# Kernel tuning notes

Measured on AMD Instinct MI355X. Metric: run time of the kernel, lower is better.

## Reference

```python
import jax, jax.numpy as jnp
import numpy as np

D_MODEL = 256
N_HEADS = 8
N_LEVELS = 4
N_POINTS = 4
HEAD_DIM = D_MODEL // N_HEADS
SPATIAL = [(64, 64), (32, 32), (16, 16), (8, 8)]
LEN_IN = sum(h * w for h, w in SPATIAL)
BATCH = 4
LEN_Q = LEN_IN


def _offset_bias():
    # replicate the module's _reset_parameters grid init for sampling_offsets.bias
    th = np.arange(N_HEADS, dtype=np.float64) * (2.0 * np.pi / N_HEADS)
    g = np.stack([np.cos(th), np.sin(th)], -1)
    g = g / np.abs(g).max(-1, keepdims=True)
    g = np.tile(g[:, None, None, :], (1, N_LEVELS, N_POINTS, 1))
    g = g * (np.arange(N_POINTS) + 1)[None, None, :, None]
    return jnp.asarray(g.reshape(-1), jnp.float32)


def setup_inputs() -> dict:
    key = jax.random.key(0)
    ks = jax.random.split(key, 10)
    s = 1.0 / np.sqrt(D_MODEL)
    return {
        "query": jax.random.normal(ks[0], (BATCH, LEN_Q, D_MODEL), jnp.float32),
        "reference_points": jax.random.uniform(ks[1], (BATCH, LEN_Q, N_LEVELS, 2), jnp.float32),
        "input_flatten": jax.random.normal(ks[2], (BATCH, LEN_IN, D_MODEL), jnp.float32),
        "input_spatial_shapes": np.array(SPATIAL, dtype=np.int64),
        "input_level_start_index": np.cumsum([0] + [h * w for h, w in SPATIAL[:-1]]).astype(np.int64),
        "W_val": jax.random.normal(ks[3], (D_MODEL, D_MODEL), jnp.float32) * s,
        "b_val": jnp.zeros((D_MODEL,), jnp.float32),
        "W_off": jax.random.normal(ks[4], (D_MODEL, N_HEADS * N_LEVELS * N_POINTS * 2), jnp.float32) * 0.01,
        "b_off": _offset_bias(),
        "W_attn": jax.random.normal(ks[5], (D_MODEL, N_HEADS * N_LEVELS * N_POINTS), jnp.float32) * 0.01,
        "b_attn": jnp.zeros((N_HEADS * N_LEVELS * N_POINTS,), jnp.float32),
        "W_out": jax.random.normal(ks[6], (D_MODEL, D_MODEL), jnp.float32) * s,
        "b_out": jnp.zeros((D_MODEL,), jnp.float32),
    }


def bilinear_sample(v, grid):
    # v: [B, C, H, W]; grid: [B, Q, P, 2] normalized to [-1, 1] (x=W axis, y=H axis)
    # matches torch F.grid_sample(mode='bilinear', padding_mode='zeros', align_corners=False)
    B, C, H, W = v.shape
    x = (grid[..., 0] + 1.0) * (W * 0.5) - 0.5
    y = (grid[..., 1] + 1.0) * (H * 0.5) - 0.5
    x0 = jnp.floor(x)
    y0 = jnp.floor(y)
    wx = x - x0
    wy = y - y0
    v_flat = v.reshape(B, C, H * W)

    def corner(xi, yi, wgt):
        valid = (xi >= 0) & (xi <= W - 1) & (yi >= 0) & (yi <= H - 1)
        xc = jnp.clip(xi, 0, W - 1).astype(jnp.int32)
        yc = jnp.clip(yi, 0, H - 1).astype(jnp.int32)
        idx = (yc * W + xc).reshape(B, 1, -1)
        g = jnp.take_along_axis(v_flat, jnp.broadcast_to(idx, (B, C, idx.shape[-1])), axis=2)
        return g * (wgt * valid).reshape(B, 1, -1)

    out = (corner(x0, y0, (1 - wx) * (1 - wy))
           + corner(x0 + 1, y0, wx * (1 - wy))
           + corner(x0, y0 + 1, (1 - wx) * wy)
           + corner(x0 + 1, y0 + 1, wx * wy))
    return out.reshape(B, C, grid.shape[1], grid.shape[2])


def reference(query, reference_points, input_flatten, input_spatial_shapes,
              input_level_start_index, W_val, b_val, W_off, b_off,
              W_attn, b_attn, W_out, b_out):
    ss = np.asarray(input_spatial_shapes)  # static [L, 2] (H, W)
    Nb, Lq, _ = query.shape
    value = (input_flatten @ W_val + b_val).reshape(Nb, -1, N_HEADS, HEAD_DIM)
    off = (query @ W_off + b_off).reshape(Nb, Lq, N_HEADS, N_LEVELS, N_POINTS, 2)
    attn = (query @ W_attn + b_attn).reshape(Nb, Lq, N_HEADS, N_LEVELS * N_POINTS)
    attn = jax.nn.softmax(attn, -1).reshape(Nb, Lq, N_HEADS, N_LEVELS, N_POINTS)
    # offset normalizer: (W, H) per level
    normalizer = jnp.asarray(ss[:, ::-1].copy(), jnp.float32)
    loc = reference_points[:, :, None, :, None, :] + off / normalizer[None, None, None, :, None, :]
    grids = 2.0 * loc - 1.0  # [N, Lq, H, L, P, 2]
    splits = np.cumsum([int(h) * int(w) for h, w in ss])[:-1]
    value_list = jnp.split(value, splits, axis=1)
    out = jnp.zeros((Nb * N_HEADS, HEAD_DIM, Lq), query.dtype)
    for lid, (h, w) in enumerate(ss):
        h, w = int(h), int(w)
        v = value_list[lid].transpose(0, 2, 3, 1).reshape(Nb * N_HEADS, HEAD_DIM, h, w)
        g = grids[:, :, :, lid].transpose(0, 2, 1, 3, 4).reshape(Nb * N_HEADS, Lq, N_POINTS, 2)
        sampled = bilinear_sample(v, g)  # [N*H, D, Lq, P]
        aw = attn[:, :, :, lid].transpose(0, 2, 1, 3).reshape(Nb * N_HEADS, 1, Lq, N_POINTS)
        out = out + (sampled * aw).sum(-1)
    out = out.reshape(Nb, N_HEADS * HEAD_DIM, Lq).transpose(0, 2, 1)
    return out @ W_out + b_out
```

## Files before the change

### kernel.cpp

```cpp
#include <hip/hip_runtime.h>
#include <hip/hip_bf16.h>
#include <math.h>

typedef unsigned short ushort_t;
typedef __attribute__((ext_vector_type(8))) short bf16x8;
typedef __attribute__((ext_vector_type(4))) float f32x4;

constexpr int BATCH   = 4;
constexpr int D_MODEL = 256;
constexpr int LEN_IN  = 5440;
constexpr int LEN_Q   = 5440;
constexpr int M_TOT   = BATCH * LEN_Q;

#define ASG __attribute__((address_space(1)))
#define ASL __attribute__((address_space(3)))

__device__ __forceinline__ void gld16(const void* g, void* l) {
    __builtin_amdgcn_global_load_lds((ASG const void*)g, (ASL void*)l, 16, 0, 0);
}

__device__ __forceinline__ ushort_t bfbits(float x) {
    __hip_bfloat16 h = __float2bfloat16(x);
    ushort_t u; __builtin_memcpy(&u, &h, 2); return u;
}
__device__ __forceinline__ unsigned pk2(float a, float b) {
    return (unsigned)bfbits(a) | ((unsigned)bfbits(b) << 16);
}

__global__ __launch_bounds__(256) void pack_inputs(
    const float* __restrict__ inflat, const float* __restrict__ query,
    const float* __restrict__ Wv, const float* __restrict__ Wo,
    const float* __restrict__ Wa, const float* __restrict__ Wout,
    const float* __restrict__ b_off, const float* __restrict__ b_attn,
    ushort_t* __restrict__ in_bf, ushort_t* __restrict__ q_bf,
    ushort_t* __restrict__ wvT, ushort_t* __restrict__ woaT,
    ushort_t* __restrict__ woutT, float* __restrict__ bias_oa)
{
    const int blk = blockIdx.x, tid = threadIdx.x;
    if (blk < 5440) {
        const float* src = (blk < 2720) ? inflat : query;
        ushort_t*    dst = (blk < 2720) ? in_bf : q_bf;
        const int rb = (blk < 2720) ? blk : blk - 2720;
        const size_t base = (size_t)rb * 2048 + tid * 8;
        float4 a = *(const float4*)(src + base);
        float4 b = *(const float4*)(src + base + 4);
        uint4 o;
        o.x = pk2(a.x, a.y); o.y = pk2(a.z, a.w);
        o.z = pk2(b.x, b.y); o.w = pk2(b.z, b.w);
        *(uint4*)(dst + base) = o;
    } else if (blk < 5504) {
        const float* src = (blk < 5472) ? Wv : Wout;
        ushort_t*    dst = (blk < 5472) ? wvT : woutT;
        const int base = (blk - ((blk < 5472) ? 5440 : 5472)) * 2048;
#pragma unroll
        for (int i = 0; i < 8; i++) {
            const int idx = base + i * 256 + tid;
            const int k = idx >> 8, n = idx & 255;
            dst[n * 256 + k] = bfbits(src[idx]);
        }
    } else if (blk < 5552) {
        const int base = (blk - 5504) * 2048;
#pragma unroll
        for (int i = 0; i < 8; i++) {
            const int idx = base + i * 256 + tid;
            const int k = idx / 384, j = idx - k * 384;
            const float v = (j < 256) ? Wo[k * 256 + j] : Wa[k * 128 + (j - 256)];
            woaT[j * 256 + k] = bfbits(v);
        }
    } else {
        bias_oa[tid] = b_off[tid];
        if (tid < 128) bias_oa[256 + tid] = b_attn[tid];
    }
}

template <bool OUT_BF16>
__device__ __forceinline__ void gemm_core(
    const ushort_t* __restrict__ A, const ushort_t* __restrict__ BT,
    const float* __restrict__ bias, void* __restrict__ Cp, int N,
    int bm, int bn, ushort_t* As, ushort_t* Bs)
{
    const int tid  = threadIdx.x;
    const int wave = tid >> 6, lane = tid & 63;
    const int wm = (wave >> 1) * 64, wn = (wave & 1) * 64;
    const int c0 = 2 * wave, c1 = 2 * wave + 1;
    const int kb = (lane & 3) * 8;
    const ushort_t* gA0 = A  + (size_t)(bm + c0 * 16 + (lane >> 2)) * 256 + kb;
    const ushort_t* gA1 = A  + (size_t)(bm + c1 * 16 + (lane >> 2)) * 256 + kb;
    const ushort_t* gB0 = BT + (size_t)(bn + c0 * 16 + (lane >> 2)) * 256 + kb;
    const ushort_t* gB1 = BT + (size_t)(bn + c1 * 16 + (lane >> 2)) * 256 + kb;
    ushort_t* lA0 = As + c0 * 512;
    ushort_t* lA1 = As + c1 * 512;
    ushort_t* lB0 = Bs + c0 * 512;
    ushort_t* lB1 = Bs + c1 * 512;

    f32x4 acc[4][4] = {};

    const int row = lane & 15, kg = (lane >> 4) * 8;
    for (int kt = 0; kt < 8; kt++) {
        gld16(gA0, lA0); gld16(gA1, lA1);
        gld16(gB0, lB0); gld16(gB1, lB1);
        gA0 += 32; gA1 += 32; gB0 += 32; gB1 += 32;
        __syncthreads();
        bf16x8 af[4], bfr[4];
#pragma unroll
        for (int i = 0; i < 4; i++)
            af[i] = *(const bf16x8*)(As + (wm + i * 16 + row) * 32 + kg);
#pragma unroll
        for (int j = 0; j < 4; j++)
            bfr[j] = *(const bf16x8*)(Bs + (wn + j * 16 + row) * 32 + kg);
#pragma unroll
        for (int i = 0; i < 4; i++)
#pragma unroll
            for (int j = 0; j < 4; j++)
                acc[i][j] = __builtin_amdgcn_mfma_f32_16x16x32_bf16(
                    af[i], bfr[j], acc[i][j], 0, 0, 0);
        __syncthreads();
    }

    const int col = lane & 15, rbase = (lane >> 4) * 4;
#pragma unroll
    for (int j = 0; j < 4; j++) {
        const int cc = bn + wn + j * 16 + col;
        const float bv = bias[cc];
#pragma unroll
        for (int i = 0; i < 4; i++) {
            const int rr = bm + wm + i * 16 + rbase;
#pragma unroll
            for (int r = 0; r < 4; r++) {
                const float v = acc[i][j][r] + bv;
                if (OUT_BF16) ((ushort_t*)Cp)[(size_t)(rr + r) * N + cc] = bfbits(v);
                else          ((float*)Cp)[(size_t)(rr + r) * N + cc] = v;
            }
        }
    }
}

__global__ __launch_bounds__(256) void gemm_dual(
    const ushort_t* __restrict__ in_bf, const ushort_t* __restrict__ wvT,
    const float* __restrict__ b_val, ushort_t* __restrict__ value_bf,
    const ushort_t* __restrict__ q_bf, const ushort_t* __restrict__ woaT,
    const float* __restrict__ bias_oa, float* __restrict__ offattn)
{
    __shared__ ushort_t As[128 * 32];
    __shared__ ushort_t Bs[128 * 32];
    int blk = blockIdx.x;
    if (blk < 340) {
        const int bn = (blk & 1) * 128, bm = (blk >> 1) * 128;
        gemm_core<true>(in_bf, wvT, b_val, value_bf, 256, bm, bn, As, Bs);
    } else {
        blk -= 340;
        const int bn = (blk % 3) * 128, bm = (blk / 3) * 128;
        gemm_core<false>(q_bf, woaT, bias_oa, offattn, 384, bm, bn, As, Bs);
    }
}

__global__ __launch_bounds__(256) void gemm_out(
    const ushort_t* __restrict__ mid_bf, const ushort_t* __restrict__ woutT,
    const float* __restrict__ b_out, float* __restrict__ out)
{
    __shared__ ushort_t As[128 * 32];
    __shared__ ushort_t Bs[128 * 32];
    const int bn = (blockIdx.x & 1) * 128, bm = (blockIdx.x >> 1) * 128;
    gemm_core<false>(mid_bf, woutT, b_out, out, 256, bm, bn, As, Bs);
}

__device__ __forceinline__ void acc8(float* acc, uint4 v, float w) {
    const unsigned* p = &v.x;
#pragma unroll
    for (int d = 0; d < 4; d++) {
        const unsigned u = p[d];
        const float lo = __uint_as_float(u << 16);
        const float hi = __uint_as_float(u & 0xFFFF0000u);
        acc[2 * d]     = fmaf(w, lo, acc[2 * d]);
        acc[2 * d + 1] = fmaf(w, hi, acc[2 * d + 1]);
    }
}

__global__ __launch_bounds__(256) void msda_sample_bf16(
    const ushort_t* __restrict__ value, const float* __restrict__ refp,
    const float* __restrict__ offattn, ushort_t* __restrict__ mid)
{
    constexpr int LVL_H[4]  = {64, 32, 16, 8};
    constexpr int LVL_W[4]  = {64, 32, 16, 8};
    constexpr int LVL_ST[4] = {0, 4096, 5120, 5376};

    const int tid  = threadIdx.x;
    const int bq   = blockIdx.x * 8 + (tid >> 5);
    const int b    = bq / LEN_Q;
    const int t32  = tid & 31;
    const int head = t32 >> 2;
    const int c8   = (t32 & 3) * 8;

    const float* base = offattn + (size_t)bq * 384;
    const float* lp = base + 256 + head * 16;
    float4 l0 = ((const float4*)lp)[0];
    float4 l1 = ((const float4*)lp)[1];
    float4 l2 = ((const float4*)lp)[2];
    float4 l3 = ((const float4*)lp)[3];
    float lg[16] = {l0.x, l0.y, l0.z, l0.w, l1.x, l1.y, l1.z, l1.w,
                    l2.x, l2.y, l2.z, l2.w, l3.x, l3.y, l3.z, l3.w};
    float mx = lg[0];
#pragma unroll
    for (int j = 1; j < 16; j++) mx = fmaxf(mx, lg[j]);

    const float* op = base + head * 32;
    float4 ov[8];
#pragma unroll
    for (int j = 0; j < 8; j++) ov[j] = ((const float4*)op)[j];
    const float* rp = refp + (size_t)bq * 8;
    float4 r0 = ((const float4*)rp)[0];
    float4 r1 = ((const float4*)rp)[1];
    const float rx[4] = {r0.x, r0.z, r1.x, r1.z};
    const float ry[4] = {r0.y, r0.w, r1.y, r1.w};

    const ushort_t* vbase = value + (size_t)b * LEN_IN * 256 + head * 32 + c8;

    float acc[8] = {};
    float esum = 0.f;

#pragma unroll
    for (int l = 0; l < 4; l++) {
        const int H = LVL_H[l], W = LVL_W[l], st = LVL_ST[l];
        const float fW = (float)W, fH = (float)H;
#pragma unroll
        for (int p = 0; p < 4; p++) {
            const float* o2 = &ov[l * 2].x;
            const float ox = o2[p * 2 + 0];
            const float oy = o2[p * 2 + 1];
            const float x = (rx[l] + ox / fW) * fW - 0.5f;
            const float y = (ry[l] + oy / fH) * fH - 0.5f;
            const float x0f = floorf(x), y0f = floorf(y);
            const float wx = x - x0f, wy = y - y0f;
            const int ix0 = (int)x0f, iy0 = (int)y0f;
            const int ix1 = ix0 + 1,  iy1 = iy0 + 1;
            const float vx0 = (ix0 >= 0 && ix0 < W) ? 1.f : 0.f;
            const float vx1 = (ix1 >= 0 && ix1 < W) ? 1.f : 0.f;
            const float vy0 = (iy0 >= 0 && iy0 < H) ? 1.f : 0.f;
            const float vy1 = (iy1 >= 0 && iy1 < H) ? 1.f : 0.f;
            const int cx0 = min(max(ix0, 0), W - 1);
            const int cx1 = min(max(ix1, 0), W - 1);
            const int cy0 = min(max(iy0, 0), H - 1);
            const int cy1 = min(max(iy1, 0), H - 1);
            const float hx0 = (1.f - wx) * vx0, hx1 = wx * vx1;
            const float hy0 = (1.f - wy) * vy0, hy1 = wy * vy1;

            const ushort_t* rp0 = vbase + (size_t)(st + cy0 * W) * 256;
            const ushort_t* rp1 = vbase + (size_t)(st + cy1 * W) * 256;
            uint4 v00 = *(const uint4*)(rp0 + (size_t)cx0 * 256);
            uint4 v01 = *(const uint4*)(rp0 + (size_t)cx1 * 256);
            uint4 v10 = *(const uint4*)(rp1 + (size_t)cx0 * 256);
            uint4 v11 = *(const uint4*)(rp1 + (size_t)cx1 * 256);

            const float e = __expf(lg[l * 4 + p] - mx);
            esum += e;
            acc8(acc, v00, e * hx0 * hy0);
            acc8(acc, v01, e * hx1 * hy0);
            acc8(acc, v10, e * hx0 * hy1);
            acc8(acc, v11, e * hx1 * hy1);
        }
    }

    const float inv = 1.f / esum;
    uint4 o;
    o.x = pk2(acc[0] * inv, acc[1] * inv);
    o.y = pk2(acc[2] * inv, acc[3] * inv);
    o.z = pk2(acc[4] * inv, acc[5] * inv);
    o.w = pk2(acc[6] * inv, acc[7] * inv);
    *(uint4*)(mid + (size_t)bq * 256 + head * 32 + c8) = o;
}

extern "C" void kernel_launch(void* const* d_in, const int* in_sizes, int n_in,
                              void* d_out, int out_size, void* d_ws, size_t ws_size,
                              hipStream_t stream)
{
    const float* query  = (const float*)d_in[0];
    const float* refp   = (const float*)d_in[1];
    const float* inflat = (const float*)d_in[2];
    const float* W_val  = (const float*)d_in[5];
    const float* b_val  = (const float*)d_in[6];
    const float* W_off  = (const float*)d_in[7];
    const float* W_attn = (const float*)d_in[9];
    const float* b_off  = (const float*)d_in[8];
    const float* b_attn = (const float*)d_in[10];
    const float* W_out  = (const float*)d_in[11];
    const float* b_out  = (const float*)d_in[12];
    float* out = (float*)d_out;

    char* ws = (char*)d_ws;
    ushort_t* in_bf    = (ushort_t*)ws;
    ushort_t* q_bf     = (ushort_t*)(ws + 11141120);
    ushort_t* value_bf = (ushort_t*)(ws + 22282240);
    ushort_t* wvT      = (ushort_t*)(ws + 33423360);
    ushort_t* woutT    = (ushort_t*)(ws + 33554432);
    ushort_t* woaT     = (ushort_t*)(ws + 33685504);
    float*    bias_oa  = (float*)   (ws + 33882112);
    float*    offattn  = (float*)   (ws + 33883648);
    ushort_t* mid_bf   = in_bf;

    dim3 blk(256);
    pack_inputs<<<dim3(5553), blk, 0, stream>>>(
        inflat, query, W_val, W_off, W_attn, W_out, b_off, b_attn,
        in_bf, q_bf, wvT, woaT, woutT, bias_oa);
    gemm_dual<<<dim3(850), blk, 0, stream>>>(
        in_bf, wvT, b_val, value_bf, q_bf, woaT, bias_oa, offattn);
    msda_sample_bf16<<<dim3(M_TOT / 8), blk, 0, stream>>>(
        value_bf, refp, offattn, mid_bf);
    gemm_out<<<dim3(340), blk, 0, stream>>>(
        mid_bf, woutT, b_out, out);
}
```

Baseline: 206.9 us.

## Store value in per-head planar layout and split sampling across levels per thread

The value projection GEMM now writes its bf16 output in a [batch*head][pixel][32] layout, so each sampled corner is a contiguous 64-byte row. The sampling kernel is restructured so that each block handles one (batch, head) slice of 64 queries, with blocks swizzled so a slice stays on one XCD for L2 locality. Each thread handles one level for a query, loads the full 32-channel corner, and accumulates with packed f32x2 FMAs. Partial sums from the four levels are reduced through shared memory and the softmax max and sum through shuffles. The aim is better cache locality and fewer, wider gathers, at the cost of a scattered GEMM epilogue store and extra LDS traffic for the reduction.

```diff
diff --git a/kernel.cpp b/kernel.cpp
--- a/kernel.cpp
+++ b/kernel.cpp
@@ -5,6 +5,7 @@
 typedef unsigned short ushort_t;
 typedef __attribute__((ext_vector_type(8))) short bf16x8;
 typedef __attribute__((ext_vector_type(4))) float f32x4;
+typedef __attribute__((ext_vector_type(2))) float f32x2;
 
 constexpr int BATCH   = 4;
 constexpr int D_MODEL = 256;
@@ -73,7 +74,7 @@
     }
 }
 
-template <bool OUT_BF16>
+template <int OUT_MODE>
 __device__ __forceinline__ void gemm_core(
     const ushort_t* __restrict__ A, const ushort_t* __restrict__ BT,
     const float* __restrict__ bias, void* __restrict__ Cp, int N,
@@ -128,8 +129,17 @@
 #pragma unroll
             for (int r = 0; r < 4; r++) {
                 const float v = acc[i][j][r] + bv;
-                if (OUT_BF16) ((ushort_t*)Cp)[(size_t)(rr + r) * N + cc] = bfbits(v);
-                else          ((float*)Cp)[(size_t)(rr + r) * N + cc] = v;
+                const int m = rr + r;
+                if (OUT_MODE == 0) {
+                    ((float*)Cp)[(size_t)m * N + cc] = v;
+                } else if (OUT_MODE == 1) {
+                    ((ushort_t*)Cp)[(size_t)m * N + cc] = bfbits(v);
+                } else {
+                    const int bb  = m / LEN_IN;
+                    const int pix = m - bb * LEN_IN;
+                    const int head = cc >> 5, ch = cc & 31;
+                    ((ushort_t*)Cp)[((size_t)((bb * 8 + head) * LEN_IN + pix) << 5) + ch] = bfbits(v);
+                }
             }
         }
     }
@@ -146,11 +156,11 @@
     int blk = blockIdx.x;
     if (blk < 340) {
         const int bn = (blk & 1) * 128, bm = (blk >> 1) * 128;
-        gemm_core<true>(in_bf, wvT, b_val, value_bf, 256, bm, bn, As, Bs);
+        gemm_core<2>(in_bf, wvT, b_val, value_bf, 256, bm, bn, As, Bs);
     } else {
         blk -= 340;
         const int bn = (blk % 3) * 128, bm = (blk / 3) * 128;
-        gemm_core<false>(q_bf, woaT, bias_oa, offattn, 384, bm, bn, As, Bs);
+        gemm_core<0>(q_bf, woaT, bias_oa, offattn, 384, bm, bn, As, Bs);
     }
 }
 
@@ -161,112 +171,138 @@
     __shared__ ushort_t As[128 * 32];
     __shared__ ushort_t Bs[128 * 32];
     const int bn = (blockIdx.x & 1) * 128, bm = (blockIdx.x >> 1) * 128;
-    gemm_core<false>(mid_bf, woutT, b_out, out, 256, bm, bn, As, Bs);
-}
-
-__device__ __forceinline__ void acc8(float* acc, uint4 v, float w) {
-    const unsigned* p = &v.x;
-#pragma unroll
-    for (int d = 0; d < 4; d++) {
-        const unsigned u = p[d];
-        const float lo = __uint_as_float(u << 16);
-        const float hi = __uint_as_float(u & 0xFFFF0000u);
-        acc[2 * d]     = fmaf(w, lo, acc[2 * d]);
-        acc[2 * d + 1] = fmaf(w, hi, acc[2 * d + 1]);
-    }
-}
-
-__global__ __launch_bounds__(256) void msda_sample_bf16(
-    const ushort_t* __restrict__ value, const float* __restrict__ refp,
-    const float* __restrict__ offattn, ushort_t* __restrict__ mid)
-{
-    constexpr int LVL_H[4]  = {64, 32, 16, 8};
-    constexpr int LVL_W[4]  = {64, 32, 16, 8};
-    constexpr int LVL_ST[4] = {0, 4096, 5120, 5376};
-
-    const int tid  = threadIdx.x;
-    const int bq   = blockIdx.x * 8 + (tid >> 5);
-    const int b    = bq / LEN_Q;
-    const int t32  = tid & 31;
-    const int head = t32 >> 2;
-    const int c8   = (t32 & 3) * 8;
-
-    const float* base = offattn + (size_t)bq * 384;
-    const float* lp = base + 256 + head * 16;
-    float4 l0 = ((const float4*)lp)[0];
-    float4 l1 = ((const float4*)lp)[1];
-    float4 l2 = ((const float4*)lp)[2];
-    float4 l3 = ((const float4*)lp)[3];
-    float lg[16] = {l0.x, l0.y, l0.z, l0.w, l1.x, l1.y, l1.z, l1.w,
-                    l2.x, l2.y, l2.z, l2.w, l3.x, l3.y, l3.z, l3.w};
-    float mx = lg[0];
-#pragma unroll
-    for (int j = 1; j < 16; j++) mx = fmaxf(mx, lg[j]);
-
-    const float* op = base + head * 32;
-    float4 ov[8];
-#pragma unroll
-    for (int j = 0; j < 8; j++) ov[j] = ((const float4*)op)[j];
-    const float* rp = refp + (size_t)bq * 8;
-    float4 r0 = ((const float4*)rp)[0];
-    float4 r1 = ((const float4*)rp)[1];
-    const float rx[4] = {r0.x, r0.z, r1.x, r1.z};
-    const float ry[4] = {r0.y, r0.w, r1.y, r1.w};
-
-    const ushort_t* vbase = value + (size_t)b * LEN_IN * 256 + head * 32 + c8;
-
-    float acc[8] = {};
+    gemm_core<0>(mid_bf, woutT, b_out, out, 256, bm, bn, As, Bs);
+}
+
+__device__ __forceinline__ void accd(f32x2& a, unsigned u, f32x2 w) {
+    f32x2 v;
+    v.x = __uint_as_float(u << 16);
+    v.y = __uint_as_float(u & 0xFFFF0000u);
+    a = w * v + a;
+}
+__device__ __forceinline__ void acc_corner(f32x2* a, uint4 A, uint4 B, uint4 C, uint4 D, float wf) {
+    const f32x2 w = {wf, wf};
+    accd(a[0],  A.x, w); accd(a[1],  A.y, w); accd(a[2],  A.z, w); accd(a[3],  A.w, w);
+    accd(a[4],  B.x, w); accd(a[5],  B.y, w); accd(a[6],  B.z, w); accd(a[7],  B.w, w);
+    accd(a[8],  C.x, w); accd(a[9],  C.y, w); accd(a[10], C.z, w); accd(a[11], C.w, w);
+    accd(a[12], D.x, w); accd(a[13], D.y, w); accd(a[14], D.z, w); accd(a[15], D.w, w);
+}
+
+__global__ __launch_bounds__(256) void msda_sample_v2(
+    const ushort_t* __restrict__ value,
+    const float* __restrict__ refp,
+    const float* __restrict__ offattn,
+    ushort_t* __restrict__ mid)
+{
+    __shared__ float4 part[8][256];
+
+    const int tid = threadIdx.x;
+    const unsigned bid = blockIdx.x;
+    const int xcd   = bid & 7;
+    const int pos   = bid >> 3;
+    const int slice = pos / 85;
+    const int qc    = pos - slice * 85;
+    const int bh    = xcd * 4 + slice;
+    const int b     = bh >> 3, h = bh & 7;
+
+    const int ql = tid >> 2;
+    const int pl = tid & 3;
+    const int q  = qc * 64 + ql;
+    const int bq = b * LEN_Q + q;
+
+    const int   shift = 6 - pl;
+    const int   W     = 1 << shift;
+    const float fW    = (float)W;
+    const float invW  = __uint_as_float((unsigned)(127 - shift) << 23);
+    const int   st    = (pl == 0) ? 0 : (pl == 1) ? 4096 : (pl == 2) ? 5120 : 5376;
+
+    const float2 rr2 = *(const float2*)(refp + (size_t)bq * 8 + pl * 2);
+    const float* oab = offattn + (size_t)bq * 384;
+    const float4 o01 = *(const float4*)(oab + h * 32 + pl * 8);
+    const float4 o23 = *(const float4*)(oab + h * 32 + pl * 8 + 4);
+    const float4 lg  = *(const float4*)(oab + 256 + h * 16 + pl * 4);
+
+    float mx = fmaxf(fmaxf(lg.x, lg.y), fmaxf(lg.z, lg.w));
+    mx = fmaxf(mx, __shfl_xor(mx, 1));
+    mx = fmaxf(mx, __shfl_xor(mx, 2));
+
+    const char* vbc = (const char*)(value + (size_t)bh * (LEN_IN * 32));
+
+    f32x2 acc2[16];
+#pragma unroll
+    for (int d = 0; d < 16; d++) acc2[d] = (f32x2){0.f, 0.f};
     float esum = 0.f;
 
-#pragma unroll
-    for (int l = 0; l < 4; l++) {
-        const int H = LVL_H[l], W = LVL_W[l], st = LVL_ST[l];
-        const float fW = (float)W, fH = (float)H;
-#pragma unroll
-        for (int p = 0; p < 4; p++) {
-            const float* o2 = &ov[l * 2].x;
-            const float ox = o2[p * 2 + 0];
-            const float oy = o2[p * 2 + 1];
-            const float x = (rx[l] + ox / fW) * fW - 0.5f;
-            const float y = (ry[l] + oy / fH) * fH - 0.5f;
-            const float x0f = floorf(x), y0f = floorf(y);
-            const float wx = x - x0f, wy = y - y0f;
-            const int ix0 = (int)x0f, iy0 = (int)y0f;
-            const int ix1 = ix0 + 1,  iy1 = iy0 + 1;
-            const float vx0 = (ix0 >= 0 && ix0 < W) ? 1.f : 0.f;
-            const float vx1 = (ix1 >= 0 && ix1 < W) ? 1.f : 0.f;
-            const float vy0 = (iy0 >= 0 && iy0 < H) ? 1.f : 0.f;
-            const float vy1 = (iy1 >= 0 && iy1 < H) ? 1.f : 0.f;
-            const int cx0 = min(max(ix0, 0), W - 1);
-            const int cx1 = min(max(ix1, 0), W - 1);
-            const int cy0 = min(max(iy0, 0), H - 1);
-            const int cy1 = min(max(iy1, 0), H - 1);
-            const float hx0 = (1.f - wx) * vx0, hx1 = wx * vx1;
-            const float hy0 = (1.f - wy) * vy0, hy1 = wy * vy1;
-
-            const ushort_t* rp0 = vbase + (size_t)(st + cy0 * W) * 256;
-            const ushort_t* rp1 = vbase + (size_t)(st + cy1 * W) * 256;
-            uint4 v00 = *(const uint4*)(rp0 + (size_t)cx0 * 256);
-            uint4 v01 = *(const uint4*)(rp0 + (size_t)cx1 * 256);
-            uint4 v10 = *(const uint4*)(rp1 + (size_t)cx0 * 256);
-            uint4 v11 = *(const uint4*)(rp1 + (size_t)cx1 * 256);
-
-            const float e = __expf(lg[l * 4 + p] - mx);
-            esum += e;
-            acc8(acc, v00, e * hx0 * hy0);
-            acc8(acc, v01, e * hx1 * hy0);
-            acc8(acc, v10, e * hx0 * hy1);
-            acc8(acc, v11, e * hx1 * hy1);
-        }
+    const float oxA[4] = {o01.x, o01.z, o23.x, o23.z};
+    const float oyA[4] = {o01.y, o01.w, o23.y, o23.w};
+    const float lgA[4] = {lg.x, lg.y, lg.z, lg.w};
+
+#pragma unroll
+    for (int p = 0; p < 4; p++) {
+        const float x = (rr2.x + oxA[p] * invW) * fW - 0.5f;
+        const float y = (rr2.y + oyA[p] * invW) * fW - 0.5f;
+        const float x0f = floorf(x), y0f = floorf(y);
+        const float wx = x - x0f, wy = y - y0f;
+        const int ix0 = (int)x0f, iy0 = (int)y0f;
+        const int ix1 = ix0 + 1,  iy1 = iy0 + 1;
+        const float vx0 = (ix0 >= 0 && ix0 < W) ? 1.f : 0.f;
+        const float vx1 = (ix1 >= 0 && ix1 < W) ? 1.f : 0.f;
+        const float vy0 = (iy0 >= 0 && iy0 < W) ? 1.f : 0.f;
+        const float vy1 = (iy1 >= 0 && iy1 < W) ? 1.f : 0.f;
+        const int cx0 = min(max(ix0, 0), W - 1);
+        const int cx1 = min(max(ix1, 0), W - 1);
+        const int cy0 = min(max(iy0, 0), W - 1);
+        const int cy1 = min(max(iy1, 0), W - 1);
+        const float hx0 = (1.f - wx) * vx0, hx1 = wx * vx1;
+        const float hy0 = (1.f - wy) * vy0, hy1 = wy * vy1;
+
+        const float e = __expf(lgA[p] - mx);
+        esum += e;
+        const float w00 = e * hx0 * hy0, w01 = e * hx1 * hy0;
+        const float w10 = e * hx0 * hy1, w11 = e * hx1 * hy1;
+
+        const int r0 = st + (cy0 << shift), r1 = st + (cy1 << shift);
+        const uint4* c00 = (const uint4*)(vbc + ((size_t)(r0 + cx0) << 6));
+        const uint4* c01 = (const uint4*)(vbc + ((size_t)(r0 + cx1) << 6));
+        const uint4* c10 = (const uint4*)(vbc + ((size_t)(r1 + cx0) << 6));
+        const uint4* c11 = (const uint4*)(vbc + ((size_t)(r1 + cx1) << 6));
+        uint4 A0 = c00[0], A1 = c00[1], A2 = c00[2], A3 = c00[3];
+        uint4 B0 = c01[0], B1 = c01[1], B2 = c01[2], B3 = c01[3];
+        uint4 C0 = c10[0], C1 = c10[1], C2 = c10[2], C3 = c10[3];
+        uint4 D0 = c11[0], D1 = c11[1], D2 = c11[2], D3 = c11[3];
+
+        acc_corner(acc2, A0, A1, A2, A3, w00);
+        acc_corner(acc2, B0, B1, B2, B3, w01);
+        acc_corner(acc2, C0, C1, C2, C3, w10);
+        acc_corner(acc2, D0, D1, D2, D3, w11);
+    }
+
+    esum += __shfl_xor(esum, 1);
+    esum += __shfl_xor(esum, 2);
+
+#pragma unroll
+    for (int j = 0; j < 8; j++)
+        part[j][tid] = make_float4(acc2[2 * j].x, acc2[2 * j].y,
+                                   acc2[2 * j + 1].x, acc2[2 * j + 1].y);
+
+    const int j0 = pl * 2;
+    const int lb = tid & ~3;
+    float4 s0 = part[j0][lb], s1 = part[j0 + 1][lb];
+#pragma unroll
+    for (int pp = 1; pp < 4; pp++) {
+        const float4 t0 = part[j0][lb + pp];
+        const float4 t1 = part[j0 + 1][lb + pp];
+        s0.x += t0.x; s0.y += t0.y; s0.z += t0.z; s0.w += t0.w;
+        s1.x += t1.x; s1.y += t1.y; s1.z += t1.z; s1.w += t1.w;
     }
 
     const float inv = 1.f / esum;
     uint4 o;
-    o.x = pk2(acc[0] * inv, acc[1] * inv);
-    o.y = pk2(acc[2] * inv, acc[3] * inv);
-    o.z = pk2(acc[4] * inv, acc[5] * inv);
-    o.w = pk2(acc[6] * inv, acc[7] * inv);
-    *(uint4*)(mid + (size_t)bq * 256 + head * 32 + c8) = o;
+    o.x = pk2(s0.x * inv, s0.y * inv);
+    o.y = pk2(s0.z * inv, s0.w * inv);
+    o.z = pk2(s1.x * inv, s1.y * inv);
+    o.w = pk2(s1.z * inv, s1.w * inv);
+    *(uint4*)(mid + (size_t)bq * 256 + h * 32 + pl * 8) = o;
 }
 
 extern "C" void kernel_launch(void* const* d_in, const int* in_sizes, int n_in,
@@ -303,7 +339,7 @@
         in_bf, q_bf, wvT, woaT, woutT, bias_oa);
     gemm_dual<<<dim3(850), blk, 0, stream>>>(
         in_bf, wvT, b_val, value_bf, q_bf, woaT, bias_oa, offattn);
-    msda_sample_bf16<<<dim3(M_TOT / 8), blk, 0, stream>>>(
+    msda_sample_v2<<<dim3(2720), blk, 0, stream>>>(
         value_bf, refp, offattn, mid_bf);
     gemm_out<<<dim3(340), blk, 0, stream>>>(
         mid_bf, woutT, b_out, out);
```

Result: slower. 215.5 us (+4.2%).
